# Kernel tuning notes

Measured on AMD Instinct MI355X. Metric: run time of the kernel, lower is better.

## Reference

```python
import jax, jax.numpy as jnp
import numpy as np

N = 16384          # input points
F = 128            # feature dim (x is (N, 3+F))
POOL = 4           # pooling_factor
M = N // POOL      # number of FPS query points
K = 16             # num_neighbors


def setup_inputs() -> dict:
    key = jax.random.key(0)
    x = jax.random.normal(key, (N, 3 + F), dtype=jnp.float32)
    return {"x": x}


def _fps(coords, m):
    """Furthest point sampling: coords (N,3) -> m indices. Deterministic start at 0."""
    n = coords.shape[0]

    def step(carry, _):
        min_d2, last = carry
        d2 = jnp.sum((coords - coords[last]) ** 2, axis=-1)  # (N,)
        min_d2 = jnp.minimum(min_d2, d2)
        nxt = jnp.argmax(min_d2).astype(jnp.int32)
        return (min_d2, nxt), nxt

    init = (jnp.full((n,), jnp.inf, dtype=coords.dtype), jnp.int32(0))
    _, idxs = jax.lax.scan(step, init, None, length=m - 1)
    return jnp.concatenate([jnp.zeros((1,), dtype=jnp.int32), idxs])


def reference(x):
    coords = x[:, :3]                          # (N,3)
    fps_idx = _fps(coords, M)                  # (M,)
    q_points = coords[fps_idx]                 # (M,3)

    # knn neighbor query: squared distances (M,N), take K nearest
    d2 = jnp.sum((q_points[:, None, :] - coords[None, :, :]) ** 2, axis=-1)
    _, nbr_idx = jax.lax.top_k(-d2, K)         # (M,K)

    s_feats = x[nbr_idx, 3:]                   # (M,K,F) gather
    pooled = jnp.max(s_feats, axis=1)          # feat_mapping='max' -> (M,F)
    return jnp.concatenate([q_points, pooled], axis=-1)  # (M, 3+F)
```

## Files before the change

kernel.cpp:

```cpp
#include <hip/hip_runtime.h>

#define N_PTS 16384
#define ROWF  131
#define M_OUT 4096
#define KNN   16
#define FPS_T 1024
#define SORT_T 1024

typedef unsigned long long u64;
typedef float f32x2 __attribute__((ext_vector_type(2)));

__device__ __constant__ unsigned short c_spread4[16] =
  {0,1,8,9,64,65,72,73,512,513,520,521,576,577,584,585};

__device__ __forceinline__ int cell_of(float x, float y, float z) {
  int ix = (int)floorf((x + 4.0f) * 2.0f); ix = ix < 0 ? 0 : (ix > 15 ? 15 : ix);
  int iy = (int)floorf((y + 4.0f) * 2.0f); iy = iy < 0 ? 0 : (iy > 15 ? 15 : iy);
  int iz = (int)floorf((z + 4.0f) * 2.0f); iz = iz < 0 ? 0 : (iz > 15 ? 15 : iz);
  return (int)c_spread4[ix] | ((int)c_spread4[iy] << 1) | ((int)c_spread4[iz] << 2);
}

template <int CTRL, int ROW_MASK>
__device__ __forceinline__ u64 kmax_dpp(u64 k) {
  const int lo = (int)(unsigned)k, hi = (int)(unsigned)(k >> 32);
  const int nlo = __builtin_amdgcn_update_dpp(lo, lo, CTRL, ROW_MASK, 0xf, false);
  const int nhi = __builtin_amdgcn_update_dpp(hi, hi, CTRL, ROW_MASK, 0xf, false);
  const u64 nk = ((u64)(unsigned)nhi << 32) | (unsigned)nlo;
  return nk > k ? nk : k;
}

__global__ void prep_kernel(const float* __restrict__ x,
                            float4* __restrict__ coords4) {
  const int p = blockIdx.x * blockDim.x + threadIdx.x;
  if (p < N_PTS) {
    coords4[p] = make_float4(x[p * ROWF + 0], x[p * ROWF + 1],
                             x[p * ROWF + 2], 0.0f);
  }
}

__global__ __launch_bounds__(1024, 1)
void sort_kernel(const float4* __restrict__ coords4, float4* __restrict__ gP4) {
  __shared__ unsigned int sh[4096];
  __shared__ unsigned int sws[16];
  const int tid = threadIdx.x, lane = tid & 63, wid = tid >> 6;

#pragma unroll
  for (int i = 0; i < 4; ++i) sh[tid * 4 + i] = 0;
  __syncthreads();

  int cel[16];
#pragma unroll
  for (int j = 0; j < 16; ++j) {
    const float4 v = coords4[tid + SORT_T * j];
    const int c = cell_of(v.x, v.y, v.z);
    cel[j] = c;
    atomicAdd(&sh[c], 1u);
  }
  __syncthreads();

  const unsigned h0 = sh[tid * 4 + 0], h1 = sh[tid * 4 + 1];
  const unsigned h2 = sh[tid * 4 + 2], h3 = sh[tid * 4 + 3];
  const unsigned tsum = h0 + h1 + h2 + h3;
  unsigned inc = tsum;
#pragma unroll
  for (int off = 1; off < 64; off <<= 1) {
    const unsigned v = __shfl_up(inc, off);
    if (lane >= off) inc += v;
  }
  if (lane == 63) sws[wid] = inc;
  __syncthreads();
  if (tid == 0) {
    unsigned run = 0;
#pragma unroll
    for (int w = 0; w < 16; ++w) { const unsigned t = sws[w]; sws[w] = run; run += t; }
  }
  __syncthreads();
  const unsigned base = sws[wid] + inc - tsum;
  sh[tid * 4 + 0] = base;
  sh[tid * 4 + 1] = base + h0;
  sh[tid * 4 + 2] = base + h0 + h1;
  sh[tid * 4 + 3] = base + h0 + h1 + h2;
  __syncthreads();

#pragma unroll
  for (int j = 0; j < 16; ++j) {
    const int p = tid + SORT_T * j;
    const float4 v = coords4[p];
    const unsigned rk = atomicAdd(&sh[cel[j]], 1u);
    const int slot = (int)(((rk & 15u) << 10) | (rk >> 4));
    gP4[slot] = make_float4(v.x, v.y, v.z, __int_as_float(p));
  }
}

#define REP16(F) F(0) F(1) F(2) F(3) F(4) F(5) F(6) F(7) \
                 F(8) F(9) F(10) F(11) F(12) F(13) F(14) F(15)
#define REP8P(F) F(0,0,1) F(1,2,3) F(2,4,5) F(3,6,7) \
                 F(4,8,9) F(5,10,11) F(6,12,13) F(7,14,15)

__global__
__attribute__((amdgpu_flat_work_group_size(FPS_T, FPS_T)))
__attribute__((amdgpu_waves_per_eu(4, 4)))
void fps_kernel(const float4* __restrict__ coords4,
                const float4* __restrict__ gP4, float* __restrict__ out) {
#pragma clang fp contract(off)
  __shared__ u64 s_wkey[2][16];
  const int tid = threadIdx.x, lane = tid & 63, wid = tid >> 6;

#define FPS_DECLP(t,a,b) f32x2 PX##t, PY##t, PZ##t;
  REP8P(FPS_DECLP)
#undef FPS_DECLP
#define FPS_DECLS(j) float md##j; unsigned ni##j;
  REP16(FPS_DECLS)
#undef FPS_DECLS

#define FPS_INITP(t,a,b) {                                                 \
    const float4 va = gP4[(a << 10) + tid];                                \
    const float4 vb = gP4[(b << 10) + tid];                                \
    PX##t = (f32x2){va.x, vb.x};                                           \
    PY##t = (f32x2){va.y, vb.y};                                           \
    PZ##t = (f32x2){va.z, vb.z};                                           \
    ni##a = (unsigned)__float_as_int(va.w);                                \
    ni##b = (unsigned)__float_as_int(vb.w);                                \
    md##a = __int_as_float(0x7f800000);                                    \
    md##b = __int_as_float(0x7f800000); }
  REP8P(FPS_INITP)
#undef FPS_INITP

  asm volatile("" : "+v"(PX0), "+v"(PY0), "+v"(PZ0), "+v"(PX1), "+v"(PY1),
                    "+v"(PZ1), "+v"(PX2), "+v"(PY2), "+v"(PZ2), "+v"(PX3),
                    "+v"(PY3), "+v"(PZ3));
  asm volatile("" : "+v"(PX4), "+v"(PY4), "+v"(PZ4), "+v"(PX5), "+v"(PY5),
                    "+v"(PZ5), "+v"(PX6), "+v"(PY6), "+v"(PZ6), "+v"(PX7),
                    "+v"(PY7), "+v"(PZ7));
  asm volatile("" : "+v"(ni0), "+v"(ni1), "+v"(ni2), "+v"(ni3), "+v"(ni4),
                    "+v"(ni5), "+v"(ni6), "+v"(ni7), "+v"(ni8), "+v"(ni9),
                    "+v"(ni10), "+v"(ni11), "+v"(ni12), "+v"(ni13),
                    "+v"(ni14), "+v"(ni15));

  float sx = 0.f, sy = 0.f, sz = 0.f;
#define FPS_ACCP(t,a,b) { sx += PX##t.x + PX##t.y;                         \
    sy += PY##t.x + PY##t.y; sz += PZ##t.x + PZ##t.y; }
  REP8P(FPS_ACCP)
#undef FPS_ACCP
  const float ccx = sx * (1.0f / 16.0f), ccy = sy * (1.0f / 16.0f),
              ccz = sz * (1.0f / 16.0f);
  float cr2 = 0.f;
#define FPS_RADP(t,a,b) {                                                  \
    const float dxa = PX##t.x - ccx, dya = PY##t.x - ccy,                  \
                dza = PZ##t.x - ccz;                                       \
    cr2 = fmaxf(cr2, dxa * dxa + dya * dya + dza * dza);                   \
    const float dxb = PX##t.y - ccx, dyb = PY##t.y - ccy,                  \
                dzb = PZ##t.y - ccz;                                       \
    cr2 = fmaxf(cr2, dxb * dxb + dyb * dyb + dzb * dzb); }
  REP8P(FPS_RADP)
#undef FPS_RADP
  const float cr = sqrtf(cr2) * 1.000001f + 1e-6f;

  float thr = __int_as_float(0x7f800000);
  u64 wkk = 0;

  const float4 q0 = coords4[0];
  float qx = q0.x, qy = q0.y, qz = q0.z;
  if (tid == 0) { out[0] = qx; out[1] = qy; out[2] = qz; }

  for (int s = 1; s < M_OUT; ++s) {
    const float dqx = qx - ccx, dqy = qy - ccy, dqz = qz - ccz;
    const float dd = dqx * dqx + dqy * dqy + dqz * dqz;
    const bool ldirty = (dd * 0.999999f <= thr);

    if (__ballot(ldirty)) {
      const f32x2 QX = {qx, qx}, QY = {qy, qy}, QZ = {qz, qz};
      float ma = 0.f, mb = 0.f;
#define FPS_UPDP(t,a,b) {                                                  \
      const f32x2 dx = PX##t - QX;                                        \
      const f32x2 dy = PY##t - QY;                                        \
      const f32x2 dz = PZ##t - QZ;                                        \
      const f32x2 xx = dx * dx;                                           \
      const f32x2 yy = dy * dy;                                           \
      const f32x2 zz = dz * dz;                                           \
      const f32x2 ss = xx + yy;                                           \
      const f32x2 d2 = ss + zz;                                           \
      const float nma = fminf(md##a, d2.x); md##a = nma;                  \
      ma = fmaxf(ma, nma);                                                \
      const float nmb = fminf(md##b, d2.y); md##b = nmb;                  \
      mb = fmaxf(mb, nmb); }
      REP8P(FPS_UPDP)
#undef FPS_UPDP
      const float m = fmaxf(ma, mb);
      unsigned c = 0xFFFFFFFFu;
#define FPS_SCAN(j) c = (md##j == m) ? (ni##j < c ? ni##j : c) : c;
      REP16(FPS_SCAN)
#undef FPS_SCAN
      u64 k = ((u64)__float_as_uint(m) << 32) | (unsigned)(N_PTS - 1 - c);

      k = kmax_dpp<0xB1,  0xf>(k);
      k = kmax_dpp<0x4E,  0xf>(k);
      k = kmax_dpp<0x141, 0xf>(k);
      k = kmax_dpp<0x140, 0xf>(k);
      k = kmax_dpp<0x142, 0xa>(k);
      k = kmax_dpp<0x143, 0xc>(k);
      wkk = k;

      const float u = (cr + sqrtf(m * 1.0001f)) * 1.000003f;
      thr = u * u * 1.000001f;
    }

    const int par = s & 1;
    if (lane == 63) s_wkey[par][wid] = wkk;
    __syncthreads();
    u64 kk = s_wkey[par][lane & 15];
    kk = kmax_dpp<0xB1,  0xf>(kk);
    kk = kmax_dpp<0x4E,  0xf>(kk);
    kk = kmax_dpp<0x141, 0xf>(kk);
    kk = kmax_dpp<0x140, 0xf>(kk);

    const int oidx = (N_PTS - 1) - (int)(unsigned)(kk & 0xFFFFFFFFu);
    const float4 wpt = coords4[oidx];
    qx = wpt.x; qy = wpt.y; qz = wpt.z;
    if (tid == 0) {
      float* orow = out + (size_t)s * ROWF;
      orow[0] = qx; orow[1] = qy; orow[2] = qz;
    }
  }
}

__global__ __launch_bounds__(256)
void knn_pool_kernel(const float* __restrict__ x,
                     const float4* __restrict__ coords4,
                     float* __restrict__ out) {
  const int lane = threadIdx.x & 63;
  const int q = blockIdx.x * 4 + (threadIdx.x >> 6);

  const float qx = out[(size_t)q * ROWF + 0];
  const float qy = out[(size_t)q * ROWF + 1];
  const float qz = out[(size_t)q * ROWF + 2];

  u64 h[KNN];
#pragma unroll
  for (int k = 0; k < KNN; ++k) h[k] = ~0ULL;

  for (int c = lane; c < N_PTS; c += 64) {
    const float4 v = coords4[c];
    const float dx = v.x - qx, dy = v.y - qy, dz = v.z - qz;
    const float d2 = __fadd_rn(__fadd_rn(__fmul_rn(dx, dx), __fmul_rn(dy, dy)),
                               __fmul_rn(dz, dz));
    const u64 e = ((u64)__float_as_uint(d2) << 32) | (unsigned)c;
    if (e < h[KNN - 1]) {
#pragma unroll
      for (int k = KNN - 1; k >= 1; --k) {
        const u64 prev = h[k - 1];
        h[k] = (e < prev) ? prev : ((e < h[k]) ? e : h[k]);
      }
      h[0] = (e < h[0]) ? e : h[0];
    }
  }

  int nbr[KNN];
#pragma unroll
  for (int rr = 0; rr < KNN; ++rr) {
    u64 best = h[0];
#pragma unroll
    for (int off = 32; off; off >>= 1) {
      const u64 o = __shfl_xor(best, off);
      best = (o < best) ? o : best;
    }
    nbr[rr] = (int)(unsigned)(best & 0xffffffffULL);
    if (h[0] == best) {
#pragma unroll
      for (int k = 0; k < KNN - 1; ++k) h[k] = h[k + 1];
      h[KNN - 1] = ~0ULL;
    }
  }

  float a0 = __int_as_float(0xff800000), a1 = a0;
#pragma unroll
  for (int rr = 0; rr < KNN; ++rr) {
    const float* row = x + (size_t)nbr[rr] * ROWF + 3;
    a0 = fmaxf(a0, row[lane]);
    a1 = fmaxf(a1, row[lane + 64]);
  }
  float* orow = out + (size_t)q * ROWF + 3;
  orow[lane] = a0;
  orow[lane + 64] = a1;
}

extern "C" void kernel_launch(void* const* d_in, const int* in_sizes, int n_in,
                              void* d_out, int out_size, void* d_ws, size_t ws_size,
                              hipStream_t stream) {
  const float* x = (const float*)d_in[0];
  float* out = (float*)d_out;

  float4* coords4 = (float4*)d_ws;
  float4* gP4     = coords4 + N_PTS;

  hipLaunchKernelGGL(prep_kernel, dim3(64), dim3(256), 0, stream, x, coords4);
  hipLaunchKernelGGL(sort_kernel, dim3(1), dim3(1024), 0, stream, coords4, gP4);
  hipLaunchKernelGGL(fps_kernel, dim3(1), dim3(FPS_T), 0, stream,
                     coords4, gP4, out);
  hipLaunchKernelGGL(knn_pool_kernel, dim3(M_OUT / 4), dim3(256), 0, stream,
                     x, coords4, out);
}
```

Before: 6.795 ms.

## Split per-wave FPS culling into four spatial sub-groups with separate bounds

The sort kernel's slot mapping changes so that each wave's 16 points per lane form four spatially coherent groups of 256 points. FPS keeps a separate centroid, radius and skip threshold per group, so a wave updates only the groups the new query point can affect instead of all 16 points whenever any is dirty. This cuts distance-update work per step but adds separate DPP max and min reductions per active group and more per-group branching.

```diff
diff --git a/kernel.cpp b/kernel.cpp
--- a/kernel.cpp
+++ b/kernel.cpp
@@ -28,6 +28,32 @@
   const u64 nk = ((u64)(unsigned)nhi << 32) | (unsigned)nlo;
   return nk > k ? nk : k;
 }
+template <int CTRL, int ROW_MASK>
+__device__ __forceinline__ float fmax_dpp(float v) {
+  const int p = __builtin_amdgcn_update_dpp(__float_as_int(v), __float_as_int(v),
+                                            CTRL, ROW_MASK, 0xf, false);
+  return fmaxf(v, __int_as_float(p));
+}
+template <int CTRL, int ROW_MASK>
+__device__ __forceinline__ unsigned umin_dpp(unsigned v) {
+  const unsigned p = (unsigned)__builtin_amdgcn_update_dpp((int)v, (int)v,
+                                            CTRL, ROW_MASK, 0xf, false);
+  return v < p ? v : p;
+}
+
+__device__ __forceinline__ float wave_fsum(float v) {
+#pragma unroll
+  for (int off = 32; off; off >>= 1) v += __shfl_xor(v, off);
+  return v;
+}
+__device__ __forceinline__ float wave_fmax(float v) {
+#pragma unroll
+  for (int off = 32; off; off >>= 1) v = fmaxf(v, __shfl_xor(v, off));
+  return v;
+}
+__device__ __forceinline__ float uni_f(float v) {
+  return __int_as_float(__builtin_amdgcn_readfirstlane(__float_as_int(v)));
+}
 
 __global__ void prep_kernel(const float* __restrict__ x,
                             float4* __restrict__ coords4) {
@@ -87,7 +113,9 @@
     const int p = tid + SORT_T * j;
     const float4 v = coords4[p];
     const unsigned rk = atomicAdd(&sh[cel[j]], 1u);
-    const int slot = (int)(((rk & 15u) << 10) | (rk >> 4));
+    const unsigned w = rk >> 10, g = (rk >> 8) & 3u,
+                   l = (rk >> 2) & 63u, jj = rk & 3u;
+    const int slot = (int)((((g << 2) | jj) << 10) | ((w << 6) | l));
     gP4[slot] = make_float4(v.x, v.y, v.z, __int_as_float(p));
   }
 }
@@ -126,83 +154,100 @@
   REP8P(FPS_INITP)
 #undef FPS_INITP
 
-  asm volatile("" : "+v"(PX0), "+v"(PY0), "+v"(PZ0), "+v"(PX1), "+v"(PY1),
-                    "+v"(PZ1), "+v"(PX2), "+v"(PY2), "+v"(PZ2), "+v"(PX3),
-                    "+v"(PY3), "+v"(PZ3));
-  asm volatile("" : "+v"(PX4), "+v"(PY4), "+v"(PZ4), "+v"(PX5), "+v"(PY5),
-                    "+v"(PZ5), "+v"(PX6), "+v"(PY6), "+v"(PZ6), "+v"(PX7),
-                    "+v"(PY7), "+v"(PZ7));
-  asm volatile("" : "+v"(ni0), "+v"(ni1), "+v"(ni2), "+v"(ni3), "+v"(ni4),
-                    "+v"(ni5), "+v"(ni6), "+v"(ni7), "+v"(ni8), "+v"(ni9),
-                    "+v"(ni10), "+v"(ni11), "+v"(ni12), "+v"(ni13),
-                    "+v"(ni14), "+v"(ni15));
-
-  float sx = 0.f, sy = 0.f, sz = 0.f;
-#define FPS_ACCP(t,a,b) { sx += PX##t.x + PX##t.y;                         \
-    sy += PY##t.x + PY##t.y; sz += PZ##t.x + PZ##t.y; }
-  REP8P(FPS_ACCP)
-#undef FPS_ACCP
-  const float ccx = sx * (1.0f / 16.0f), ccy = sy * (1.0f / 16.0f),
-              ccz = sz * (1.0f / 16.0f);
-  float cr2 = 0.f;
-#define FPS_RADP(t,a,b) {                                                  \
-    const float dxa = PX##t.x - ccx, dya = PY##t.x - ccy,                  \
-                dza = PZ##t.x - ccz;                                       \
-    cr2 = fmaxf(cr2, dxa * dxa + dya * dya + dza * dza);                   \
-    const float dxb = PX##t.y - ccx, dyb = PY##t.y - ccy,                  \
-                dzb = PZ##t.y - ccz;                                       \
-    cr2 = fmaxf(cr2, dxb * dxb + dyb * dyb + dzb * dzb); }
-  REP8P(FPS_RADP)
-#undef FPS_RADP
-  const float cr = sqrtf(cr2) * 1.000001f + 1e-6f;
-
-  float thr = __int_as_float(0x7f800000);
+#define GDECL(g) float gcx##g, gcy##g, gcz##g, gr##g, gthr##g; u64 gk##g;
+  GDECL(0) GDECL(1) GDECL(2) GDECL(3)
+#undef GDECL
+
+#define GINIT(g, tA, tB) {                                                 \
+    const float sx = wave_fsum(PX##tA.x + PX##tA.y + PX##tB.x + PX##tB.y); \
+    const float sy = wave_fsum(PY##tA.x + PY##tA.y + PY##tB.x + PY##tB.y); \
+    const float sz = wave_fsum(PZ##tA.x + PZ##tA.y + PZ##tB.x + PZ##tB.y); \
+    gcx##g = uni_f(sx * (1.0f / 256.0f));                                  \
+    gcy##g = uni_f(sy * (1.0f / 256.0f));                                  \
+    gcz##g = uni_f(sz * (1.0f / 256.0f));                                  \
+    float r2 = 0.f;                                                        \
+    { const float dx = PX##tA.x - gcx##g, dy = PY##tA.x - gcy##g,          \
+                  dz = PZ##tA.x - gcz##g;                                  \
+      r2 = fmaxf(r2, dx * dx + dy * dy + dz * dz); }                       \
+    { const float dx = PX##tA.y - gcx##g, dy = PY##tA.y - gcy##g,          \
+                  dz = PZ##tA.y - gcz##g;                                  \
+      r2 = fmaxf(r2, dx * dx + dy * dy + dz * dz); }                       \
+    { const float dx = PX##tB.x - gcx##g, dy = PY##tB.x - gcy##g,          \
+                  dz = PZ##tB.x - gcz##g;                                  \
+      r2 = fmaxf(r2, dx * dx + dy * dy + dz * dz); }                       \
+    { const float dx = PX##tB.y - gcx##g, dy = PY##tB.y - gcy##g,          \
+                  dz = PZ##tB.y - gcz##g;                                  \
+      r2 = fmaxf(r2, dx * dx + dy * dy + dz * dz); }                       \
+    r2 = wave_fmax(r2);                                                    \
+    gr##g   = uni_f(sqrtf(r2) * 1.000001f + 1e-6f);                        \
+    gthr##g = uni_f(__int_as_float(0x7f800000));                           \
+    gk##g   = 0; }
+  GINIT(0, 0, 1) GINIT(1, 2, 3) GINIT(2, 4, 5) GINIT(3, 6, 7)
+#undef GINIT
+
   u64 wkk = 0;
-
   const float4 q0 = coords4[0];
   float qx = q0.x, qy = q0.y, qz = q0.z;
   if (tid == 0) { out[0] = qx; out[1] = qy; out[2] = qz; }
 
   for (int s = 1; s < M_OUT; ++s) {
-    const float dqx = qx - ccx, dqy = qy - ccy, dqz = qz - ccz;
-    const float dd = dqx * dqx + dqy * dqy + dqz * dqz;
-    const bool ldirty = (dd * 0.999999f <= thr);
-
-    if (__ballot(ldirty)) {
-      const f32x2 QX = {qx, qx}, QY = {qy, qy}, QZ = {qz, qz};
-      float ma = 0.f, mb = 0.f;
-#define FPS_UPDP(t,a,b) {                                                  \
-      const f32x2 dx = PX##t - QX;                                        \
-      const f32x2 dy = PY##t - QY;                                        \
-      const f32x2 dz = PZ##t - QZ;                                        \
-      const f32x2 xx = dx * dx;                                           \
-      const f32x2 yy = dy * dy;                                           \
-      const f32x2 zz = dz * dz;                                           \
-      const f32x2 ss = xx + yy;                                           \
-      const f32x2 d2 = ss + zz;                                           \
-      const float nma = fminf(md##a, d2.x); md##a = nma;                  \
-      ma = fmaxf(ma, nma);                                                \
-      const float nmb = fminf(md##b, d2.y); md##b = nmb;                  \
-      mb = fmaxf(mb, nmb); }
-      REP8P(FPS_UPDP)
-#undef FPS_UPDP
-      const float m = fmaxf(ma, mb);
-      unsigned c = 0xFFFFFFFFu;
-#define FPS_SCAN(j) c = (md##j == m) ? (ni##j < c ? ni##j : c) : c;
-      REP16(FPS_SCAN)
-#undef FPS_SCAN
-      u64 k = ((u64)__float_as_uint(m) << 32) | (unsigned)(N_PTS - 1 - c);
-
-      k = kmax_dpp<0xB1,  0xf>(k);
-      k = kmax_dpp<0x4E,  0xf>(k);
-      k = kmax_dpp<0x141, 0xf>(k);
-      k = kmax_dpp<0x140, 0xf>(k);
-      k = kmax_dpp<0x142, 0xa>(k);
-      k = kmax_dpp<0x143, 0xc>(k);
-      wkk = k;
-
-      const float u = (cr + sqrtf(m * 1.0001f)) * 1.000003f;
-      thr = u * u * 1.000001f;
+    const f32x2 QX = {qx, qx}, QY = {qy, qy}, QZ = {qz, qz};
+    bool any = false;
+
+#define GSTEP(g, tA, tB, e0, e1, e2, e3) {                                 \
+    const float ddx = qx - gcx##g, ddy = qy - gcy##g, ddz = qz - gcz##g;   \
+    const float dd = ddx * ddx + ddy * ddy + ddz * ddz;                    \
+    if (__builtin_amdgcn_readfirstlane(                                    \
+            (int)(dd * 0.999999f <= gthr##g))) {                          \
+      any = true;                                                          \
+      const f32x2 dxA = PX##tA - QX, dyA = PY##tA - QY, dzA = PZ##tA - QZ; \
+      const f32x2 xxA = dxA * dxA, yyA = dyA * dyA, zzA = dzA * dzA;       \
+      const f32x2 d2A = (xxA + yyA) + zzA;                                 \
+      const f32x2 dxB = PX##tB - QX, dyB = PY##tB - QY, dzB = PZ##tB - QZ; \
+      const f32x2 xxB = dxB * dxB, yyB = dyB * dyB, zzB = dzB * dzB;       \
+      const f32x2 d2B = (xxB + yyB) + zzB;                                 \
+      const float n0 = fminf(md##e0, d2A.x); md##e0 = n0;                  \
+      const float n1 = fminf(md##e1, d2A.y); md##e1 = n1;                  \
+      const float n2 = fminf(md##e2, d2B.x); md##e2 = n2;                  \
+      const float n3 = fminf(md##e3, d2B.y); md##e3 = n3;                  \
+      float gm = fmaxf(fmaxf(n0, n1), fmaxf(n2, n3));                      \
+      gm = fmax_dpp<0xB1,  0xf>(gm);                                       \
+      gm = fmax_dpp<0x4E,  0xf>(gm);                                       \
+      gm = fmax_dpp<0x141, 0xf>(gm);                                       \
+      gm = fmax_dpp<0x140, 0xf>(gm);                                       \
+      gm = fmax_dpp<0x142, 0xa>(gm);                                       \
+      gm = fmax_dpp<0x143, 0xc>(gm);                                       \
+      const float gmu = __int_as_float(                                    \
+          __builtin_amdgcn_readlane(__float_as_int(gm), 63));              \
+      unsigned c = 0xFFFFFFFFu;                                            \
+      c = (md##e0 == gmu) ? (ni##e0 < c ? ni##e0 : c) : c;                 \
+      c = (md##e1 == gmu) ? (ni##e1 < c ? ni##e1 : c) : c;                 \
+      c = (md##e2 == gmu) ? (ni##e2 < c ? ni##e2 : c) : c;                 \
+      c = (md##e3 == gmu) ? (ni##e3 < c ? ni##e3 : c) : c;                 \
+      c = umin_dpp<0xB1,  0xf>(c);                                         \
+      c = umin_dpp<0x4E,  0xf>(c);                                         \
+      c = umin_dpp<0x141, 0xf>(c);                                         \
+      c = umin_dpp<0x140, 0xf>(c);                                         \
+      c = umin_dpp<0x142, 0xa>(c);                                         \
+      c = umin_dpp<0x143, 0xc>(c);                                         \
+      const unsigned cu = (unsigned)__builtin_amdgcn_readlane((int)c, 63); \
+      gk##g = ((u64)__float_as_uint(gmu) << 32) |                          \
+              (unsigned)(N_PTS - 1 - cu);                                  \
+      const float uu = (gr##g + sqrtf(gmu * 1.0001f)) * 1.000003f;         \
+      gthr##g = uni_f(uu * uu * 1.000001f);                                \
+    } }
+    GSTEP(0, 0, 1,  0,  1,  2,  3)
+    GSTEP(1, 2, 3,  4,  5,  6,  7)
+    GSTEP(2, 4, 5,  8,  9, 10, 11)
+    GSTEP(3, 6, 7, 12, 13, 14, 15)
+#undef GSTEP
+
+    if (any) {
+      u64 w = gk0;
+      w = (gk1 > w) ? gk1 : w;
+      w = (gk2 > w) ? gk2 : w;
+      w = (gk3 > w) ? gk3 : w;
+      wkk = w;
     }
 
     const int par = s & 1;
```

Measured after the change: 8.415 ms. +23.8%, slower.
